# Optimization experiments

Hardware: AMD Instinct MI355X
Metric: run time of the kernel (lower is better)

## Reference

```python
import jax, jax.numpy as jnp
import numpy as np

V = 8000; TZ = 128; TU = 256; B = 64; H = 1024; E = 512; DG = 64
GI = E + 2 * H + DG  # GRU input size = embed + z_ctx + u_ctx + degree


def _build_sparse_z(rng):
    # faithful vectorized version of get_sparse_selective_input (minus vocab SLOT branch)
    z_np = rng.integers(0, V + 10, size=(TZ, B))  # some ids >= V -> OOV copy path
    res = np.full((TZ, B, V + TZ), 1e-10, np.float32)
    w = z_np[:-1]                                   # [TZ-1, B]
    cond = (w == 2) | (w >= V)
    ti, bi = np.meshgrid(np.arange(TZ - 1), np.arange(B), indexing='ij')
    col = np.where(cond, V + ti, w)
    val = np.where(cond, np.float32(5.0), np.float32(1.0))
    res[ti + 1, bi, col] = val
    return jnp.asarray(res.transpose(1, 0, 2))      # [B, TZ, V+TZ]


def setup_inputs():
    key = jax.random.key(0)
    ks = jax.random.split(key, 16)
    s = 0.02
    iv = 1.0 / np.sqrt(H)
    return dict(
        z_enc_out=jax.random.normal(ks[0], (TZ, B, H), jnp.float32),
        u_enc_out=jax.random.normal(ks[1], (TU, B, H), jnp.float32),
        m_t_input=jax.random.randint(ks[2], (1, B), 0, V),
        degree_input=jax.random.normal(ks[3], (B, DG), jnp.float32),
        last_hidden=jax.random.normal(ks[4], (1, B, H), jnp.float32),
        sparse_z_input=_build_sparse_z(np.random.default_rng(0)),
        emb_W=jax.random.normal(ks[5], (V, E), jnp.float32) * s,
        attn_z_W=jax.random.normal(ks[6], (H, 2 * H), jnp.float32) * s,
        attn_z_b=jnp.zeros((H,), jnp.float32),
        attn_z_v=jax.random.normal(ks[7], (H,), jnp.float32) * iv,
        attn_u_W=jax.random.normal(ks[8], (H, 2 * H), jnp.float32) * s,
        attn_u_b=jnp.zeros((H,), jnp.float32),
        attn_u_v=jax.random.normal(ks[9], (H,), jnp.float32) * iv,
        gru_Wih=jax.random.normal(ks[10], (3 * H, GI), jnp.float32) * s,
        gru_Whh=jax.random.normal(ks[11], (3 * H, H), jnp.float32) * s,
        gru_bih=jnp.zeros((3 * H,), jnp.float32),
        gru_bhh=jnp.zeros((3 * H,), jnp.float32),
        proj_W=jax.random.normal(ks[12], (V, 3 * H), jnp.float32) * s,
        proj_b=jnp.zeros((V,), jnp.float32),
        copy2_W=jax.random.normal(ks[13], (H, H), jnp.float32) * s,
        copy2_b=jnp.zeros((H,), jnp.float32),
    )


def _attn(hidden, enc, W, b, v):
    # hidden [1,B,H], enc [T,B,H] -> context [1,B,H] (Bahdanau additive attention)
    enc_b = jnp.transpose(enc, (1, 0, 2))                       # [B,T,H]
    Hrep = jnp.broadcast_to(jnp.transpose(hidden, (1, 0, 2)), enc_b.shape)
    energy = jnp.tanh(jnp.concatenate([Hrep, enc_b], -1) @ W.T + b)  # [B,T,H]
    scores = jnp.einsum('bth,h->bt', energy, v)[:, None, :]    # [B,1,T]
    alpha = jax.nn.softmax(scores, axis=2)
    ctx = jnp.einsum('bit,bth->bih', alpha, enc_b)              # [B,1,H]
    return jnp.transpose(ctx, (1, 0, 2))                        # [1,B,H]


def _gru_step(x, h, Wih, Whh, bih, bhh):
    # single step, torch gate order (r, z, n)
    gi = x @ Wih.T + bih
    gh = h @ Whh.T + bhh
    ir, iz, inn = jnp.split(gi, 3, -1)
    hr, hz, hn = jnp.split(gh, 3, -1)
    r = jax.nn.sigmoid(ir + hr)
    z = jax.nn.sigmoid(iz + hz)
    n = jnp.tanh(inn + r * hn)
    return (1.0 - z) * n + z * h


def reference(z_enc_out, u_enc_out, m_t_input, degree_input, last_hidden,
              sparse_z_input, emb_W, attn_z_W, attn_z_b, attn_z_v,
              attn_u_W, attn_u_b, attn_u_v, gru_Wih, gru_Whh, gru_bih, gru_bhh,
              proj_W, proj_b, copy2_W, copy2_b):
    m_embed = emb_W[m_t_input]                                  # [1,B,E]
    z_ctx = _attn(last_hidden, z_enc_out, attn_z_W, attn_z_b, attn_z_v)  # [1,B,H]
    u_ctx = _attn(last_hidden, u_enc_out, attn_u_W, attn_u_b, attn_u_v)  # [1,B,H]
    gru_in = jnp.concatenate([m_embed, u_ctx, z_ctx, degree_input[None]], axis=2)
    gru_out = _gru_step(gru_in, last_hidden, gru_Wih, gru_Whh, gru_bih, gru_bhh)
    new_hidden = gru_out                                        # single-layer GRU, 1 step
    gen_score = (jnp.concatenate([z_ctx, u_ctx, gru_out], 2) @ proj_W.T + proj_b)[0]  # [B,V]
    # pointer copy scores over z encoder states
    z_cs = jnp.tanh(jnp.transpose(z_enc_out, (1, 0, 2)) @ copy2_W.T + copy2_b)  # [B,TZ,H]
    z_cs = jnp.einsum('bth,bh->bt', z_cs, gru_out[0])           # [B,TZ]
    m = jnp.max(z_cs, axis=1, keepdims=True)
    e = jnp.exp(z_cs - m)
    z_copy = jnp.log(jnp.einsum('bt,btv->bv', e, sparse_z_input)) + m  # [B,V+TZ]
    scores = jax.nn.softmax(jnp.concatenate([gen_score, z_copy], axis=1), axis=1)
    gen_s, zc = scores[:, :V], scores[:, V:]
    proba = jnp.concatenate([gen_s + zc[:, :V], zc[:, V:]], axis=1)  # [B, V+TZ]
    return (proba, new_hidden, gru_out)
```

## Files before the change

### kernel.cpp

```cpp
#include <hip/hip_runtime.h>
#include <cmath>

#define B64 64
#define H 1024
#define E 512
#define DG 64
#define GIN 2624
#define TZ 128
#define TU 256
#define V 8000
#define VT 8128
#define NC 16128

using bf16x8 = __attribute__((ext_vector_type(8))) short;
using f32x4  = __attribute__((ext_vector_type(4))) float;

__device__ inline unsigned pack2(float a, float b) {
    unsigned ua = __float_as_uint(a) + 0x8000u;
    unsigned ub = __float_as_uint(b) + 0x8000u;
    return __builtin_amdgcn_perm(ub, ua, 0x07060302u);
}
__device__ inline uint2 pack4(float4 v) {
    return make_uint2(pack2(v.x, v.y), pack2(v.z, v.w));
}

__device__ inline float fast_tanh(float x) {
    float e = __expf(2.f * x);
    return 1.f - 2.f / (e + 1.f);
}
__device__ inline float fast_sig(float x) {
    return 1.f / (1.f + __expf(-x));
}

__device__ inline void gl_lds16(const void* gptr, void* lptr) {
    __builtin_amdgcn_global_load_lds(
        (const __attribute__((address_space(1))) void*)gptr,
        (__attribute__((address_space(3))) void*)lptr, 16, 0, 0);
}

__global__ void k_cvt_all(const float* __restrict__ u_enc, const float* __restrict__ z_enc,
                          const float* __restrict__ azW, const float* __restrict__ auW,
                          const float* __restrict__ c2W,
                          unsigned short* __restrict__ ubf, unsigned short* __restrict__ zbf,
                          unsigned short* __restrict__ azWbf, unsigned short* __restrict__ auWbf,
                          unsigned short* __restrict__ c2Wbf)
{
    int n = blockIdx.x, k4 = threadIdx.x * 4;
    const float* src; unsigned short* dst; int ld, koff, r;
    if (n < 16384)      { src = u_enc; dst = ubf;   ld = 1024; koff = 0;    r = n; }
    else if (n < 24576) { src = z_enc; dst = zbf;   ld = 1024; koff = 0;    r = n - 16384; }
    else if (n < 25600) { src = azW;   dst = azWbf; ld = 2048; koff = 1024; r = n - 24576; }
    else if (n < 26624) { src = auW;   dst = auWbf; ld = 2048; koff = 1024; r = n - 25600; }
    else                { src = c2W;   dst = c2Wbf; ld = 1024; koff = 0;    r = n - 26624; }
    float4 v = *(const float4*)(src + (size_t)r * ld + koff + k4);
    *(uint2*)(dst + (size_t)r * 1024 + k4) = pack4(v);
}

__global__ __launch_bounds__(256) void fused_tanh_dot_bf(
    const unsigned short* __restrict__ A,
    const unsigned short* __restrict__ W,
    const float* __restrict__ addv, int add_stride,
    const float* __restrict__ multv, int mult_stride,
    float* __restrict__ outs)
{
    __shared__ unsigned short As[128 * 32];
    __shared__ unsigned short Bs[128 * 32];
    const int tid  = threadIdx.x;
    const int wave = tid >> 6, lane = tid & 63;
    const int wm = wave >> 1, wn = wave & 1;
    const int q = lane >> 4, l16 = lane & 15;
    const int m0 = blockIdx.x * 128;
    const int n0 = blockIdx.y * 128;
    const int lrow = lane >> 2;
    const int lk   = (lane & 3) * 8;

    f32x4 acc[4][4];
#pragma unroll
    for (int i = 0; i < 4; ++i)
#pragma unroll
        for (int j = 0; j < 4; ++j) acc[i][j] = f32x4{0.f, 0.f, 0.f, 0.f};

    for (int kt = 0; kt < 32; ++kt) {
        const int k0 = kt * 32;
        __syncthreads();
#pragma unroll
        for (int j = 0; j < 2; ++j) {
            int r0 = (wave * 2 + j) * 16;
            gl_lds16(A + (size_t)(m0 + r0 + lrow) * 1024 + k0 + lk, &As[r0 * 32]);
            gl_lds16(W + (size_t)(n0 + r0 + lrow) * 1024 + k0 + lk, &Bs[r0 * 32]);
        }
        __syncthreads();
        bf16x8 af[4], bfr[4];
#pragma unroll
        for (int t = 0; t < 4; ++t) af[t]  = *(bf16x8*)&As[(wm * 64 + t * 16 + l16) * 32 + q * 8];
#pragma unroll
        for (int t = 0; t < 4; ++t) bfr[t] = *(bf16x8*)&Bs[(wn * 64 + t * 16 + l16) * 32 + q * 8];
#pragma unroll
        for (int tm = 0; tm < 4; ++tm)
#pragma unroll
            for (int tn = 0; tn < 4; ++tn)
                acc[tm][tn] = __builtin_amdgcn_mfma_f32_16x16x32_bf16(
                    af[tm], bfr[tn], acc[tm][tn], 0, 0, 0);
    }

#pragma unroll
    for (int tm = 0; tm < 4; ++tm) {
#pragma unroll
        for (int r = 0; r < 4; ++r) {
            int R = m0 + wm * 64 + tm * 16 + q * 4 + r;
            int b = R & 63;
            float s = 0.f;
#pragma unroll
            for (int tn = 0; tn < 4; ++tn) {
                int col = n0 + wn * 64 + tn * 16 + l16;
                float e = acc[tm][tn][r] + addv[(size_t)b * add_stride + col];
                s += fast_tanh(e) * multv[(size_t)b * mult_stride + col];
            }
            s += __shfl_xor(s, 1);
            s += __shfl_xor(s, 2);
            s += __shfl_xor(s, 4);
            s += __shfl_xor(s, 8);
            if (l16 == 0) atomicAdd(&outs[R], s);
        }
    }
}

__global__ __launch_bounds__(256) void ftd_z_combo(
    const unsigned short* __restrict__ A,
    const unsigned short* __restrict__ Wz,
    const float* __restrict__ hbz, const float* __restrict__ azv,
    float* __restrict__ scores,
    const unsigned short* __restrict__ Wc,
    const float* __restrict__ c2b,
    float* __restrict__ tz)
{
    __shared__ unsigned short As[128 * 32];
    __shared__ unsigned short Bs[128 * 32];
    const int tid  = threadIdx.x;
    const int wave = tid >> 6, lane = tid & 63;
    const int wm = wave >> 1, wn = wave & 1;
    const int q = lane >> 4, l16 = lane & 15;
    const int m0 = blockIdx.x * 128;
    const bool isz = blockIdx.y < 8;
    const int n0 = (isz ? blockIdx.y : blockIdx.y - 8) * 128;
    const unsigned short* W = isz ? Wz : Wc;
    const int lrow = lane >> 2;
    const int lk   = (lane & 3) * 8;

    f32x4 acc[4][4];
#pragma unroll
    for (int i = 0; i < 4; ++i)
#pragma unroll
        for (int j = 0; j < 4; ++j) acc[i][j] = f32x4{0.f, 0.f, 0.f, 0.f};

    for (int kt = 0; kt < 32; ++kt) {
        const int k0 = kt * 32;
        __syncthreads();
#pragma unroll
        for (int j = 0; j < 2; ++j) {
            int r0 = (wave * 2 + j) * 16;
            gl_lds16(A + (size_t)(m0 + r0 + lrow) * 1024 + k0 + lk, &As[r0 * 32]);
            gl_lds16(W + (size_t)(n0 + r0 + lrow) * 1024 + k0 + lk, &Bs[r0 * 32]);
        }
        __syncthreads();
        bf16x8 af[4], bfr[4];
#pragma unroll
        for (int t = 0; t < 4; ++t) af[t]  = *(bf16x8*)&As[(wm * 64 + t * 16 + l16) * 32 + q * 8];
#pragma unroll
        for (int t = 0; t < 4; ++t) bfr[t] = *(bf16x8*)&Bs[(wn * 64 + t * 16 + l16) * 32 + q * 8];
#pragma unroll
        for (int tm = 0; tm < 4; ++tm)
#pragma unroll
            for (int tn = 0; tn < 4; ++tn)
                acc[tm][tn] = __builtin_amdgcn_mfma_f32_16x16x32_bf16(
                    af[tm], bfr[tn], acc[tm][tn], 0, 0, 0);
    }

    if (isz) {
#pragma unroll
        for (int tm = 0; tm < 4; ++tm) {
#pragma unroll
            for (int r = 0; r < 4; ++r) {
                int R = m0 + wm * 64 + tm * 16 + q * 4 + r;
                int b = R & 63;
                float s = 0.f;
#pragma unroll
                for (int tn = 0; tn < 4; ++tn) {
                    int col = n0 + wn * 64 + tn * 16 + l16;
                    float e = acc[tm][tn][r] + hbz[(size_t)b * 1024 + col];
                    s += fast_tanh(e) * azv[col];
                }
                s += __shfl_xor(s, 1);
                s += __shfl_xor(s, 2);
                s += __shfl_xor(s, 4);
                s += __shfl_xor(s, 8);
                if (l16 == 0) atomicAdd(&scores[R], s);
            }
        }
    } else {
#pragma unroll
        for (int tm = 0; tm < 4; ++tm) {
#pragma unroll
            for (int r = 0; r < 4; ++r) {
                int R = m0 + wm * 64 + tm * 16 + q * 4 + r;
#pragma unroll
                for (int tn = 0; tn < 4; ++tn) {
                    int col = n0 + wn * 64 + tn * 16 + l16;
                    tz[(size_t)R * 1024 + col] = fast_tanh(acc[tm][tn][r] + c2b[col]);
                }
            }
        }
    }
}

__global__ __launch_bounds__(256) void gemm_bt_mfma(
    const float* __restrict__ A, int lda,
    const float* __restrict__ W, int ldw, int koff,
    const float* __restrict__ bias,
    float* __restrict__ C, int N,
    int ks_total, int ks_chunk)
{
    __shared__ short As[64][40];
    __shared__ short Bs[64][40];
    const int tid  = threadIdx.x;
    const int wave = tid >> 6, lane = tid & 63;
    const int wm = wave >> 1, wn = wave & 1;
    const int q = lane >> 4, l16 = lane & 15;
    const int n0 = blockIdx.x * 64;
    const int kb = blockIdx.y * ks_chunk;
    const int ke = min(kb + ks_chunk, ks_total);

    f32x4 acc[2][2];
#pragma unroll
    for (int i = 0; i < 2; ++i)
#pragma unroll
        for (int j = 0; j < 2; ++j) acc[i][j] = f32x4{0.f, 0.f, 0.f, 0.f};

    for (int ks = kb; ks < ke; ++ks) {
        const int k0 = ks * 32;
        __syncthreads();
#pragma unroll
        for (int i = 0; i < 2; ++i) {
            int slot = i * 256 + tid;
            int row  = slot >> 3;
            int kq   = (slot & 7) << 2;
            float4 a = *(const float4*)(A + (size_t)row * lda + k0 + kq);
            *(uint2*)&As[row][kq] = pack4(a);
            float4 w = *(const float4*)(W + (size_t)(n0 + row) * ldw + koff + k0 + kq);
            *(uint2*)&Bs[row][kq] = pack4(w);
        }
        __syncthreads();
        bf16x8 af[2], bfr[2];
#pragma unroll
        for (int t = 0; t < 2; ++t) af[t]  = *(bf16x8*)&As[wm * 32 + t * 16 + l16][q * 8];
#pragma unroll
        for (int t = 0; t < 2; ++t) bfr[t] = *(bf16x8*)&Bs[wn * 32 + t * 16 + l16][q * 8];
#pragma unroll
        for (int tm = 0; tm < 2; ++tm)
#pragma unroll
            for (int tn = 0; tn < 2; ++tn)
                acc[tm][tn] = __builtin_amdgcn_mfma_f32_16x16x32_bf16(
                    af[tm], bfr[tn], acc[tm][tn], 0, 0, 0);
    }

#pragma unroll
    for (int tm = 0; tm < 2; ++tm) {
#pragma unroll
        for (int r = 0; r < 4; ++r) {
            int b = wm * 32 + tm * 16 + q * 4 + r;
#pragma unroll
            for (int tn = 0; tn < 2; ++tn) {
                int n = n0 + wn * 32 + tn * 16 + l16;
                float v = acc[tm][tn][r];
                if (blockIdx.y == 0) v += bias[n];
                atomicAdd(&C[(size_t)b * N + n], v);
            }
        }
    }
}

__global__ void k_gather(const int* __restrict__ mt, const float* __restrict__ embW,
                         const float* __restrict__ degree, float* __restrict__ x)
{
    int b = blockIdx.x, tid = threadIdx.x;
    int m = mt[b];
    for (int k = tid; k < E; k += 128) x[(size_t)b * GIN + k] = embW[(size_t)m * E + k];
    if (tid < DG) x[(size_t)b * GIN + E + 2 * H + tid] = degree[b * DG + tid];
}

__global__ __launch_bounds__(256) void k_softmax_ctx_bf(
    const float* __restrict__ scores, const unsigned short* __restrict__ encbf, int T,
    float* __restrict__ x, int xoff, float* __restrict__ y, int yoff)
{
    __shared__ float red[256];
    __shared__ float al[256];
    int b = blockIdx.x, hc = blockIdx.y, tid = threadIdx.x;
    float s = (tid < T) ? scores[tid * B64 + b] : -1e30f;
    red[tid] = s; __syncthreads();
    for (int off = 128; off > 0; off >>= 1) {
        if (tid < off) red[tid] = fmaxf(red[tid], red[tid + off]);
        __syncthreads();
    }
    float mx = red[0]; __syncthreads();
    float e = (tid < T) ? __expf(s - mx) : 0.f;
    red[tid] = e; __syncthreads();
    for (int off = 128; off > 0; off >>= 1) {
        if (tid < off) red[tid] += red[tid + off];
        __syncthreads();
    }
    float inv = 1.f / red[0];
    al[tid] = e * inv;
    __syncthreads();
    int h = hc * 512 + tid * 2;
    float a0 = 0.f, a1 = 0.f;
    for (int t = 0; t < T; ++t) {
        unsigned u = *(const unsigned*)(encbf + ((size_t)t * B64 + b) * 1024 + h);
        float w = al[t];
        a0 += w * __uint_as_float(u << 16);
        a1 += w * __uint_as_float(u & 0xffff0000u);
    }
    x[(size_t)b * GIN + xoff + h]     = a0;
    x[(size_t)b * GIN + xoff + h + 1] = a1;
    y[(size_t)b * 3072 + yoff + h]     = a0;
    y[(size_t)b * 3072 + yoff + h + 1] = a1;
}

__global__ void k_gate(const float* __restrict__ gi, const float* __restrict__ gh,
                       const float* __restrict__ h0, float* __restrict__ gru,
                       float* __restrict__ y, float* __restrict__ out_hid,
                       float* __restrict__ out_gru)
{
    int b = blockIdx.x, tid = threadIdx.x;
    for (int j = tid; j < H; j += 256) {
        float ir = gi[(size_t)b * 3072 + j];
        float iz = gi[(size_t)b * 3072 + H + j];
        float in_ = gi[(size_t)b * 3072 + 2 * H + j];
        float hr = gh[(size_t)b * 3072 + j];
        float hz = gh[(size_t)b * 3072 + H + j];
        float hn = gh[(size_t)b * 3072 + 2 * H + j];
        float r = fast_sig(ir + hr);
        float z = fast_sig(iz + hz);
        float n = fast_tanh(in_ + r * hn);
        float h = h0[(size_t)b * H + j];
        float o = (1.f - z) * n + z * h;
        gru[(size_t)b * H + j] = o;
        y[(size_t)b * 3072 + 2 * H + j] = o;
        out_hid[(size_t)b * H + j] = o;
        out_gru[(size_t)b * H + j] = o;
    }
}

__global__ __launch_bounds__(512) void k_zcs_expw(
    const float* __restrict__ tz, const float* __restrict__ gru,
    float* __restrict__ ew, float* __restrict__ mb)
{
    __shared__ float g[1024];
    __shared__ float srow[TZ];
    __shared__ float red[64];
    int b = blockIdx.x, tid = threadIdx.x;
    int wave = tid >> 6, lane = tid & 63;
    for (int i = tid; i < 1024; i += 512) g[i] = gru[(size_t)b * 1024 + i];
    __syncthreads();
    float gr[16];
#pragma unroll
    for (int j = 0; j < 16; ++j) gr[j] = g[lane * 16 + j];
    for (int t = wave; t < TZ; t += 8) {
        const float* row = tz + ((size_t)t * B64 + b) * 1024 + lane * 16;
        float s = 0.f;
#pragma unroll
        for (int c = 0; c < 4; ++c) {
            float4 v = *(const float4*)(row + c * 4);
            s += v.x * gr[c * 4 + 0] + v.y * gr[c * 4 + 1]
               + v.z * gr[c * 4 + 2] + v.w * gr[c * 4 + 3];
        }
#pragma unroll
        for (int off = 32; off > 0; off >>= 1) s += __shfl_xor(s, off);
        if (lane == 0) srow[t] = s;
    }
    __syncthreads();
    if (tid < 64) red[tid] = fmaxf(srow[tid], srow[tid + 64]);
    __syncthreads();
    if (tid < 64) {
        float m = red[tid];
#pragma unroll
        for (int off = 32; off > 0; off >>= 1) m = fmaxf(m, __shfl_xor(m, off));
        red[tid] = m;
    }
    __syncthreads();
    float m = red[0];
    if (tid < TZ) ew[b * TZ + tid] = __expf(srow[tid] - m);
    if (tid == 0) mb[b] = m;
}

__global__ __launch_bounds__(256) void k_sparse(
    const float* __restrict__ sz, const float* __restrict__ ew,
    const float* __restrict__ mb, float* __restrict__ zcopy)
{
    __shared__ float es[TZ];
    int c = blockIdx.x, b = blockIdx.y, tid = threadIdx.x;
    if (tid < TZ) es[tid] = ew[b * TZ + tid];
    __syncthreads();
    if (tid >= 254) return;
    int v4 = c * 254 + tid;
    const float4* base = (const float4*)(sz + (size_t)b * TZ * VT);
    float4 acc = make_float4(0.f, 0.f, 0.f, 0.f);
    for (int t = 0; t < TZ; ++t) {
        float4 xv = base[(size_t)t * (VT / 4) + v4];
        float e = es[t];
        acc.x += e * xv.x; acc.y += e * xv.y; acc.z += e * xv.z; acc.w += e * xv.w;
    }
    float m = mb[b];
    int v = v4 * 4;
    zcopy[(size_t)b * VT + v + 0] = __logf(acc.x) + m;
    zcopy[(size_t)b * VT + v + 1] = __logf(acc.y) + m;
    zcopy[(size_t)b * VT + v + 2] = __logf(acc.z) + m;
    zcopy[(size_t)b * VT + v + 3] = __logf(acc.w) + m;
}

__global__ __launch_bounds__(1024) void k_final(
    const float* __restrict__ gen, const float* __restrict__ zcopy,
    float* __restrict__ proba)
{
    __shared__ float lg[NC];
    __shared__ float wred[16];
    int b = blockIdx.x, tid = threadIdx.x;
    int lane = tid & 63, wave = tid >> 6;
    for (int i = tid; i < V; i += 1024) lg[i] = gen[(size_t)b * V + i];
    for (int i = tid; i < VT; i += 1024) lg[V + i] = zcopy[(size_t)b * VT + i];
    __syncthreads();
    float mx = -1e30f;
    for (int i = tid; i < NC; i += 1024) mx = fmaxf(mx, lg[i]);
#pragma unroll
    for (int off = 32; off > 0; off >>= 1) mx = fmaxf(mx, __shfl_xor(mx, off));
    if (lane == 0) wred[wave] = mx;
    __syncthreads();
    mx = wred[0];
#pragma unroll
    for (int w = 1; w < 16; ++w) mx = fmaxf(mx, wred[w]);
    __syncthreads();
    float sm = 0.f;
    for (int i = tid; i < NC; i += 1024) sm += __expf(lg[i] - mx);
#pragma unroll
    for (int off = 32; off > 0; off >>= 1) sm += __shfl_xor(sm, off);
    if (lane == 0) wred[wave] = sm;
    __syncthreads();
    float Z = 0.f;
#pragma unroll
    for (int w = 0; w < 16; ++w) Z += wred[w];
    float invZ = 1.f / Z;
    for (int v = tid; v < VT; v += 1024) {
        float p = __expf(lg[V + v] - mx) * invZ;
        if (v < V) p += __expf(lg[v] - mx) * invZ;
        proba[(size_t)b * VT + v] = p;
    }
}

extern "C" void kernel_launch(void* const* d_in, const int* in_sizes, int n_in,
                              void* d_out, int out_size, void* d_ws, size_t ws_size,
                              hipStream_t stream)
{
    const float* z_enc  = (const float*)d_in[0];
    const float* u_enc  = (const float*)d_in[1];
    const int*   mt     = (const int*)d_in[2];
    const float* degree = (const float*)d_in[3];
    const float* h0     = (const float*)d_in[4];
    const float* sz     = (const float*)d_in[5];
    const float* embW   = (const float*)d_in[6];
    const float* azW    = (const float*)d_in[7];
    const float* azb    = (const float*)d_in[8];
    const float* azv    = (const float*)d_in[9];
    const float* auW    = (const float*)d_in[10];
    const float* aub    = (const float*)d_in[11];
    const float* auv    = (const float*)d_in[12];
    const float* Wih    = (const float*)d_in[13];
    const float* Whh    = (const float*)d_in[14];
    const float* bih    = (const float*)d_in[15];
    const float* bhh    = (const float*)d_in[16];
    const float* pW     = (const float*)d_in[17];
    const float* pb     = (const float*)d_in[18];
    const float* c2W    = (const float*)d_in[19];
    const float* c2b    = (const float*)d_in[20];

    float* ws       = (float*)d_ws;
    float* scores_z = ws;
    float* scores_u = ws + 8192;
    float* hbz      = ws + 32768;
    float* hbu      = ws + 98304;
    float* gi       = ws + 163840;
    float* gh       = ws + 360448;
    float* gen      = ws + 557056;
    float* x        = ws + 1069056;
    float* y        = ws + 1236992;
    float* gru      = ws + 1433600;
    float* ew       = ws + 1499136;
    float* mb       = ws + 1507328;
    float* zcopy    = ws + 1507392;
    float* tz       = ws + 2027584;
    unsigned short* ubf   = (unsigned short*)(ws + 2027584 + 8388608);
    unsigned short* zbf   = ubf + (size_t)16384 * 1024;
    unsigned short* azWbf = zbf + (size_t)8192 * 1024;
    unsigned short* auWbf = azWbf + (size_t)1024 * 1024;
    unsigned short* c2Wbf = auWbf + (size_t)1024 * 1024;

    float* out_proba = (float*)d_out;
    float* out_hid   = out_proba + (size_t)B64 * VT;
    float* out_gru   = out_hid + (size_t)B64 * H;

    hipMemsetAsync(ws, 0, 1069056 * sizeof(float), stream);

    k_cvt_all<<<27648, 256, 0, stream>>>(u_enc, z_enc, azW, auW, c2W,
                                         ubf, zbf, azWbf, auWbf, c2Wbf);

    gemm_bt_mfma<<<dim3(16, 4), 256, 0, stream>>>(h0, 1024, azW, 2048, 0, azb, hbz, 1024, 32, 8);
    gemm_bt_mfma<<<dim3(16, 4), 256, 0, stream>>>(h0, 1024, auW, 2048, 0, aub, hbu, 1024, 32, 8);
    k_gather<<<64, 128, 0, stream>>>(mt, embW, degree, x);
    gemm_bt_mfma<<<dim3(48, 4), 256, 0, stream>>>(h0, 1024, Whh, 1024, 0, bhh, gh, 3072, 32, 8);

    ftd_z_combo<<<dim3(64, 16), 256, 0, stream>>>(zbf, azWbf, hbz, azv, scores_z,
                                                  c2Wbf, c2b, tz);
    fused_tanh_dot_bf<<<dim3(128, 8), 256, 0, stream>>>(ubf, auWbf, hbu, 1024, auv, 0, scores_u);

    k_softmax_ctx_bf<<<dim3(64, 2), 256, 0, stream>>>(scores_z, zbf, TZ, x, 1536, y, 0);
    k_softmax_ctx_bf<<<dim3(64, 2), 256, 0, stream>>>(scores_u, ubf, TU, x, 512, y, 1024);

    gemm_bt_mfma<<<dim3(48, 4), 256, 0, stream>>>(x, GIN, Wih, GIN, 0, bih, gi, 3072, 82, 21);
    k_gate<<<64, 256, 0, stream>>>(gi, gh, h0, gru, y, out_hid, out_gru);

    k_zcs_expw<<<64, 512, 0, stream>>>(tz, gru, ew, mb);

    gemm_bt_mfma<<<dim3(125, 3), 256, 0, stream>>>(y, 3072, pW, 3072, 0, pb, gen, 8000, 96, 32);

    k_sparse<<<dim3(8, 64), 256, 0, stream>>>(sz, ew, mb, zcopy);

    k_final<<<64, 1024, 0, stream>>>(gen, zcopy, out_proba);
}
```

Baseline: 815.3 us.

## Increase split-K parallelism, split z-copy dot kernel, and tune sparse loads

Raises the split-K factor for all the MFMA GEMM launches to 8, so there are more blocks with fewer K tiles each. The z copy-score kernel is split into a 4-way parallel dot kernel plus a separate small softmax max/exp kernel. The sparse accumulation loop gets unrolling and nontemporal loads, and the context loop gets an unroll pragma. Together these aim to fill more compute units and hide memory latency, at the cost of more atomic accumulation traffic and an extra kernel launch.

```diff
diff --git a/kernel.cpp b/kernel.cpp
--- a/kernel.cpp
+++ b/kernel.cpp
@@ -313,6 +313,7 @@
     __syncthreads();
     int h = hc * 512 + tid * 2;
     float a0 = 0.f, a1 = 0.f;
+#pragma unroll 4
     for (int t = 0; t < T; ++t) {
         unsigned u = *(const unsigned*)(encbf + ((size_t)t * B64 + b) * 1024 + h);
         float w = al[t];
@@ -350,21 +351,22 @@
     }
 }
 
-__global__ __launch_bounds__(512) void k_zcs_expw(
+__global__ __launch_bounds__(512) void k_zcs_dot(
     const float* __restrict__ tz, const float* __restrict__ gru,
-    float* __restrict__ ew, float* __restrict__ mb)
+    float* __restrict__ zraw)
 {
     __shared__ float g[1024];
-    __shared__ float srow[TZ];
-    __shared__ float red[64];
-    int b = blockIdx.x, tid = threadIdx.x;
+    int b = blockIdx.x, quarter = blockIdx.y, tid = threadIdx.x;
     int wave = tid >> 6, lane = tid & 63;
     for (int i = tid; i < 1024; i += 512) g[i] = gru[(size_t)b * 1024 + i];
     __syncthreads();
     float gr[16];
 #pragma unroll
     for (int j = 0; j < 16; ++j) gr[j] = g[lane * 16 + j];
-    for (int t = wave; t < TZ; t += 8) {
+    int t0 = quarter * 32;
+#pragma unroll
+    for (int i = 0; i < 4; ++i) {
+        int t = t0 + wave + i * 8;
         const float* row = tz + ((size_t)t * B64 + b) * 1024 + lane * 16;
         float s = 0.f;
 #pragma unroll
@@ -375,20 +377,23 @@
         }
 #pragma unroll
         for (int off = 32; off > 0; off >>= 1) s += __shfl_xor(s, off);
-        if (lane == 0) srow[t] = s;
-    }
-    __syncthreads();
-    if (tid < 64) red[tid] = fmaxf(srow[tid], srow[tid + 64]);
-    __syncthreads();
-    if (tid < 64) {
-        float m = red[tid];
-#pragma unroll
-        for (int off = 32; off > 0; off >>= 1) m = fmaxf(m, __shfl_xor(m, off));
-        red[tid] = m;
-    }
-    __syncthreads();
-    float m = red[0];
-    if (tid < TZ) ew[b * TZ + tid] = __expf(srow[tid] - m);
+        if (lane == 0) zraw[b * TZ + t] = s;
+    }
+}
+
+__global__ void k_expw(const float* __restrict__ zraw,
+                       float* __restrict__ ew, float* __restrict__ mb)
+{
+    __shared__ float r2[2];
+    int b = blockIdx.x, tid = threadIdx.x;
+    float s = zraw[b * TZ + tid];
+    float m = s;
+#pragma unroll
+    for (int off = 32; off > 0; off >>= 1) m = fmaxf(m, __shfl_xor(m, off));
+    if ((tid & 63) == 0) r2[tid >> 6] = m;
+    __syncthreads();
+    m = fmaxf(r2[0], r2[1]);
+    ew[b * TZ + tid] = __expf(s - m);
     if (tid == 0) mb[b] = m;
 }
 
@@ -402,12 +407,13 @@
     __syncthreads();
     if (tid >= 254) return;
     int v4 = c * 254 + tid;
-    const float4* base = (const float4*)(sz + (size_t)b * TZ * VT);
+    const f32x4* base = (const f32x4*)(sz + (size_t)b * TZ * VT);
     float4 acc = make_float4(0.f, 0.f, 0.f, 0.f);
+#pragma unroll 16
     for (int t = 0; t < TZ; ++t) {
-        float4 xv = base[(size_t)t * (VT / 4) + v4];
+        f32x4 xv = __builtin_nontemporal_load(&base[(size_t)t * (VT / 4) + v4]);
         float e = es[t];
-        acc.x += e * xv.x; acc.y += e * xv.y; acc.z += e * xv.z; acc.w += e * xv.w;
+        acc.x += e * xv[0]; acc.y += e * xv[1]; acc.z += e * xv[2]; acc.w += e * xv[3];
     }
     float m = mb[b];
     int v = v4 * 4;
@@ -501,6 +507,7 @@
     unsigned short* azWbf = zbf + (size_t)8192 * 1024;
     unsigned short* auWbf = azWbf + (size_t)1024 * 1024;
     unsigned short* c2Wbf = auWbf + (size_t)1024 * 1024;
+    float* zraw = ws + 24571968;
 
     float* out_proba = (float*)d_out;
     float* out_hid   = out_proba + (size_t)B64 * VT;
@@ -511,10 +518,10 @@
     k_cvt_all<<<27648, 256, 0, stream>>>(u_enc, z_enc, azW, auW, c2W,
                                          ubf, zbf, azWbf, auWbf, c2Wbf);
 
-    gemm_bt_mfma<<<dim3(16, 4), 256, 0, stream>>>(h0, 1024, azW, 2048, 0, azb, hbz, 1024, 32, 8);
-    gemm_bt_mfma<<<dim3(16, 4), 256, 0, stream>>>(h0, 1024, auW, 2048, 0, aub, hbu, 1024, 32, 8);
+    gemm_bt_mfma<<<dim3(16, 8), 256, 0, stream>>>(h0, 1024, azW, 2048, 0, azb, hbz, 1024, 32, 4);
+    gemm_bt_mfma<<<dim3(16, 8), 256, 0, stream>>>(h0, 1024, auW, 2048, 0, aub, hbu, 1024, 32, 4);
     k_gather<<<64, 128, 0, stream>>>(mt, embW, degree, x);
-    gemm_bt_mfma<<<dim3(48, 4), 256, 0, stream>>>(h0, 1024, Whh, 1024, 0, bhh, gh, 3072, 32, 8);
+    gemm_bt_mfma<<<dim3(48, 8), 256, 0, stream>>>(h0, 1024, Whh, 1024, 0, bhh, gh, 3072, 32, 4);
 
     ftd_z_combo<<<dim3(64, 16), 256, 0, stream>>>(zbf, azWbf, hbz, azv, scores_z,
                                                   c2Wbf, c2b, tz);
@@ -523,12 +530,13 @@
     k_softmax_ctx_bf<<<dim3(64, 2), 256, 0, stream>>>(scores_z, zbf, TZ, x, 1536, y, 0);
     k_softmax_ctx_bf<<<dim3(64, 2), 256, 0, stream>>>(scores_u, ubf, TU, x, 512, y, 1024);
 
-    gemm_bt_mfma<<<dim3(48, 4), 256, 0, stream>>>(x, GIN, Wih, GIN, 0, bih, gi, 3072, 82, 21);
+    gemm_bt_mfma<<<dim3(48, 8), 256, 0, stream>>>(x, GIN, Wih, GIN, 0, bih, gi, 3072, 82, 11);
     k_gate<<<64, 256, 0, stream>>>(gi, gh, h0, gru, y, out_hid, out_gru);
 
-    k_zcs_expw<<<64, 512, 0, stream>>>(tz, gru, ew, mb);
-
-    gemm_bt_mfma<<<dim3(125, 3), 256, 0, stream>>>(y, 3072, pW, 3072, 0, pb, gen, 8000, 96, 32);
+    k_zcs_dot<<<dim3(64, 4), 512, 0, stream>>>(tz, gru, zraw);
+    k_expw<<<64, 128, 0, stream>>>(zraw, ew, mb);
+
+    gemm_bt_mfma<<<dim3(125, 8), 256, 0, stream>>>(y, 3072, pW, 3072, 0, pb, gen, 8000, 96, 12);
 
     k_sparse<<<dim3(8, 64), 256, 0, stream>>>(sz, ew, mb, zcopy);
 
```

After: 806.7 us. No clear change (-1.0%).
